# Kernel optimization log

Measured on AMD Instinct MI355X. Metric: run time of the kernel, lower is better.

## Reference

```python
import jax, jax.numpy as jnp
import numpy as np

B, T, F = 4096, 64, 32
U1, U2 = 256, 128  # stacked GRU: rnn_units, rnn_units // 2


def _gru_layer(x, Wg, bg, Wc, bc, units):
    """TF GRUCell semantics over a full sequence.
    x: [B, T, D]. Wg: [D+U, 2U], Wc: [D+U, U]. Returns outputs [B, T, U].
    r,u = sigmoid([x,h] Wg + bg); c = tanh([x, r*h] Wc + bc); h' = u*h + (1-u)*c
    """
    xT = jnp.swapaxes(x, 0, 1)  # [T, B, D]
    h0 = jnp.zeros((x.shape[0], units), x.dtype)

    def step(h, xt):
        gates = jax.nn.sigmoid(jnp.concatenate([xt, h], axis=-1) @ Wg + bg)
        r, u = jnp.split(gates, 2, axis=-1)
        c = jnp.tanh(jnp.concatenate([xt, r * h], axis=-1) @ Wc + bc)
        h_new = u * h + (1.0 - u) * c
        return h_new, h_new

    _, outs = jax.lax.scan(step, h0, xT)
    return jnp.swapaxes(outs, 0, 1)  # [B, T, U]


def setup_inputs() -> dict:
    key = jax.random.key(0)
    ks = jax.random.split(key, 12)
    s = 0.1
    inp = {
        "frames": jax.random.normal(ks[0], (B, T, F), jnp.float32),
        "W1_g": jax.random.normal(ks[1], (F + U1, 2 * U1), jnp.float32) * s,
        "b1_g": jnp.ones((2 * U1,), jnp.float32),  # TF gate bias init = 1.0
        "W1_c": jax.random.normal(ks[2], (F + U1, U1), jnp.float32) * s,
        "b1_c": jnp.zeros((U1,), jnp.float32),
        "W2_g": jax.random.normal(ks[3], (U1 + U2, 2 * U2), jnp.float32) * s,
        "b2_g": jnp.ones((2 * U2,), jnp.float32),
        "W2_c": jax.random.normal(ks[4], (U1 + U2, U2), jnp.float32) * s,
        "b2_c": jnp.zeros((U2,), jnp.float32),
        "Wd": jax.random.normal(ks[5], (U2, F), jnp.float32) * s,
        "bd": jnp.zeros((F,), jnp.float32),
    }
    return inp


def reference(frames, W1_g, b1_g, W1_c, b1_c, W2_g, b2_g, W2_c, b2_c, Wd, bd):
    # stacked GRU: MultiRNNCell([GRUCell(U1), GRUCell(U1 // 2)])
    h1 = _gru_layer(frames, W1_g, b1_g, W1_c, b1_c, U1)   # [B, T, U1]
    h2 = _gru_layer(h1, W2_g, b2_g, W2_c, b2_c, U2)       # [B, T, U2]
    last = h2[:, -1]                                       # use_cell_state=False -> outputs[:, -1]
    predicted = last @ Wd + bd                             # dense to sensor_count
    return predicted
```

## Files before the change

kernel.cpp:

```cpp
#include <hip/hip_runtime.h>


typedef unsigned short u16;
typedef __attribute__((ext_vector_type(8))) short bhalf8;
typedef __attribute__((ext_vector_type(4))) float fx4;

constexpr int Bc = 4096, Tc = 64, Fc = 32, U1 = 256, U2 = 128;
constexpr int K1 = Fc + U1;
constexpr int K2 = U1 + U2;
constexpr int NB = 16, NTHR = 512;
constexpr int LD1 = K1 + 8;
constexpr int LD2 = K2 + 8;

constexpr int nW1g = K1 * 512, nW1c = K1 * 256, nW2g = K2 * 256, nW2c = K2 * 128;
constexpr int oW1g = 0;
constexpr int oW1c = oW1g + nW1g;
constexpr int oW2g = oW1c + nW1c;
constexpr int oW2c = oW2g + nW2g;
constexpr int WTOT = oW2c + nW2c;
constexpr int nWdT = Fc * U2;

#define LGKM_BARRIER() asm volatile("s_waitcnt lgkmcnt(0)\n\ts_barrier" ::: "memory")

__device__ __forceinline__ u16 bf16_rne(float x) {
  unsigned u = __float_as_uint(x);
  return (u16)((u + 0x7fffu + ((u >> 16) & 1u)) >> 16);
}
__device__ __forceinline__ float bf16_f(u16 h) {
  return __uint_as_float(((unsigned)h) << 16);
}
__device__ __forceinline__ float sigm(float x) { return 1.0f / (1.0f + __expf(-x)); }
__device__ __forceinline__ float tanh_(float x) {
  x = fminf(fmaxf(x, -15.0f), 15.0f);
  const float s = __expf(2.0f * x);
  return (s - 1.0f) / (s + 1.0f);
}

__global__ void prep_weights(const float* __restrict__ W1g, const float* __restrict__ W1c,
                             const float* __restrict__ W2g, const float* __restrict__ W2c,
                             const float* __restrict__ Wd, u16* __restrict__ ws) {
  int j = blockIdx.x * 256 + threadIdx.x;
  if (j >= WTOT + nWdT) return;
  if (j >= WTOT) {
    const int jj = j - WTOT;
    float* wdT = (float*)(ws + WTOT);
    const int o = jj >> 7, c = jj & 127;
    wdT[jj] = Wd[c * Fc + o];
    return;
  }
  const float* src; u16* dst; int K, N, jj;
  if (j < nW1g)                    { src = W1g; K = K1; N = 512; jj = j;                      dst = ws + oW1g; }
  else if (j < nW1g + nW1c)        { src = W1c; K = K1; N = 256; jj = j - nW1g;               dst = ws + oW1c; }
  else if (j < nW1g + nW1c + nW2g) { src = W2g; K = K2; N = 256; jj = j - nW1g - nW1c;        dst = ws + oW2g; }
  else                             { src = W2c; K = K2; N = 128; jj = j - nW1g - nW1c - nW2g; dst = ws + oW2c; }
  int n = jj / K, k = jj - n * K;
  dst[(size_t)n * K + k] = bf16_rne(src[(size_t)k * N + n]);
}

template <int NT, int D>
struct Pipe {
  const u16* wp[NT];
  bhalf8 bb[D][NT];
  __device__ __forceinline__ void init(const u16* __restrict__ W, const int* n0,
                                       int K, int lc, int ao) {
#pragma unroll
    for (int i = 0; i < NT; ++i) wp[i] = W + (size_t)(n0[i] + lc) * K + ao;
  }
  __device__ __forceinline__ void prefetch() {
#pragma unroll
    for (int d = 0; d < D; ++d)
#pragma unroll
      for (int i = 0; i < NT; ++i) bb[d][i] = *(const bhalf8*)(wp[i] + d * 32);
  }
  template <int KT, int LDA>
  __device__ __forceinline__ void mm(fx4 (&acc)[NT], const u16 (&Ah)[16][LDA],
                                     const u16 (&Al)[16][LDA], int lc, int ao) {
#pragma unroll
    for (int kt = 0; kt < KT; ++kt) {
      const int k0 = kt * 32;
      const bhalf8 a_h = *(const bhalf8*)&Ah[lc][k0 + ao];
      const bhalf8 a_l = *(const bhalf8*)&Al[lc][k0 + ao];
#pragma unroll
      for (int i = 0; i < NT; ++i) {
        acc[i] = __builtin_amdgcn_mfma_f32_16x16x32_bf16(a_h, bb[kt % D][i], acc[i], 0, 0, 0);
        acc[i] = __builtin_amdgcn_mfma_f32_16x16x32_bf16(a_l, bb[kt % D][i], acc[i], 0, 0, 0);
      }
      if (kt + D < KT) {
#pragma unroll
        for (int i = 0; i < NT; ++i) bb[kt % D][i] = *(const bhalf8*)(wp[i] + (kt + D) * 32);
      }
    }
  }
};

__global__ __launch_bounds__(NTHR, 2)
void gru_mfma(const float* __restrict__ frames, const u16* __restrict__ ws,
              const float* __restrict__ b1g, const float* __restrict__ b1c,
              const float* __restrict__ b2g, const float* __restrict__ b2c,
              const float* __restrict__ bd, float* __restrict__ out) {
  __shared__ alignas(16) u16 A1h[16][LD1], A1l[16][LD1];
  __shared__ alignas(16) u16 A2h[16][LD2], A2l[16][LD2];

  const int tid = threadIdx.x;
  const int w = tid >> 6;
  const int l = tid & 63;
  const int lc = l & 15;
  const int lk = l >> 4;
  const int ao = lk * 8;
  const int row0 = lk * 4;
  const int b0 = blockIdx.x * NB;

  const float bg1r0 = b1g[w * 32 + lc],       bg1r1 = b1g[w * 32 + 16 + lc];
  const float bg1u0 = b1g[256 + w * 32 + lc], bg1u1 = b1g[256 + w * 32 + 16 + lc];
  const float bc10  = b1c[w * 32 + lc],       bc11  = b1c[w * 32 + 16 + lc];
  const float bg2r  = b2g[w * 16 + lc],       bg2u  = b2g[128 + w * 16 + lc];
  const float bc2v  = b2c[w * 16 + lc];

  Pipe<4, 4> pG1;  Pipe<2, 4> pC1;  Pipe<2, 4> pG2;  Pipe<1, 4> pC2;
  const int n0g1[4] = {w * 32, w * 32 + 16, 256 + w * 32, 256 + w * 32 + 16};
  const int n0c1[2] = {w * 32, w * 32 + 16};
  const int n0g2[2] = {w * 16, 128 + w * 16};
  const int n0c2[1] = {w * 16};
  pG1.init(ws + oW1g, n0g1, K1, lc, ao);
  pC1.init(ws + oW1c, n0c1, K1, lc, ao);
  pG2.init(ws + oW2g, n0g2, K2, lc, ao);
  pC2.init(ws + oW2c, n0c2, K2, lc, ao);

  for (int i = tid; i < 16 * LD1; i += NTHR) { (&A1h[0][0])[i] = 0; (&A1l[0][0])[i] = 0; }
  for (int i = tid; i < 16 * LD2; i += NTHR) { (&A2h[0][0])[i] = 0; (&A2l[0][0])[i] = 0; }

  const int xb = tid >> 5, xf = tid & 31;
  const float* fptr = frames + (size_t)(b0 + xb) * (Tc * Fc) + xf;

  {
    const float x0 = fptr[0];
    const u16 h = bf16_rne(x0);
    A1h[xb][xf] = h;
    A1l[xb][xf] = bf16_rne(x0 - bf16_f(h));
  }
  pG1.prefetch();
  LGKM_BARRIER();

  for (int t = 0; t < Tc; ++t) {
    const float xnxt = (t + 1 < Tc) ? fptr[(t + 1) * Fc] : 0.0f;

    fx4 acc[4] = { {bg1r0, bg1r0, bg1r0, bg1r0}, {bg1r1, bg1r1, bg1r1, bg1r1},
                   {bg1u0, bg1u0, bg1u0, bg1u0}, {bg1u1, bg1u1, bg1u1, bg1u1} };
    pG1.mm<9, LD1>(acc, A1h, A1l, lc, ao);
    pC1.prefetch();

    float hold1[2][4];
#pragma unroll
    for (int i = 0; i < 2; ++i)
#pragma unroll
      for (int q = 0; q < 4; ++q) {
        const int row = row0 + q, col = w * 32 + i * 16 + lc;
        hold1[i][q] = bf16_f(A1h[row][Fc + col]) + bf16_f(A1l[row][Fc + col]);
      }
    float rr[2][4], uu[2][4];
#pragma unroll
    for (int i = 0; i < 2; ++i)
#pragma unroll
      for (int q = 0; q < 4; ++q) { rr[i][q] = sigm(acc[i][q]); uu[i][q] = sigm(acc[2 + i][q]); }
    LGKM_BARRIER();

#pragma unroll
    for (int i = 0; i < 2; ++i)
#pragma unroll
      for (int q = 0; q < 4; ++q) {
        const int row = row0 + q, col = w * 32 + i * 16 + lc;
        const float rh = rr[i][q] * hold1[i][q];
        const u16 hh = bf16_rne(rh);
        A1h[row][Fc + col] = hh;
        A1l[row][Fc + col] = bf16_rne(rh - bf16_f(hh));
      }
    LGKM_BARRIER();

    fx4 accc[2] = { {bc10, bc10, bc10, bc10}, {bc11, bc11, bc11, bc11} };
    pC1.mm<9, LD1>(accc, A1h, A1l, lc, ao);
    pG2.prefetch();

    float hn1[2][4]; u16 hh1[2][4], hl1[2][4];
#pragma unroll
    for (int i = 0; i < 2; ++i)
#pragma unroll
      for (int q = 0; q < 4; ++q) {
        const float c = tanh_(accc[i][q]);
        const float hn = c + uu[i][q] * (hold1[i][q] - c);
        hh1[i][q] = bf16_rne(hn);
        hl1[i][q] = bf16_rne(hn - bf16_f(hh1[i][q]));
      }
    LGKM_BARRIER();
#pragma unroll
    for (int i = 0; i < 2; ++i)
#pragma unroll
      for (int q = 0; q < 4; ++q) {
        const int row = row0 + q, col = w * 32 + i * 16 + lc;
        A1h[row][Fc + col] = hh1[i][q];  A1l[row][Fc + col] = hl1[i][q];
        A2h[row][col] = hh1[i][q];       A2l[row][col] = hl1[i][q];
      }
    LGKM_BARRIER();

    fx4 acc2[2] = { {bg2r, bg2r, bg2r, bg2r}, {bg2u, bg2u, bg2u, bg2u} };
    pG2.mm<12, LD2>(acc2, A2h, A2l, lc, ao);
    pC2.prefetch();

    float hold2[4];
#pragma unroll
    for (int q = 0; q < 4; ++q) {
      const int row = row0 + q, col = w * 16 + lc;
      hold2[q] = bf16_f(A2h[row][U1 + col]) + bf16_f(A2l[row][U1 + col]);
    }
    float rr2[4], uu2[4];
#pragma unroll
    for (int q = 0; q < 4; ++q) { rr2[q] = sigm(acc2[0][q]); uu2[q] = sigm(acc2[1][q]); }
    LGKM_BARRIER();

#pragma unroll
    for (int q = 0; q < 4; ++q) {
      const int row = row0 + q, col = w * 16 + lc;
      const float rh = rr2[q] * hold2[q];
      const u16 hh = bf16_rne(rh);
      A2h[row][U1 + col] = hh;
      A2l[row][U1 + col] = bf16_rne(rh - bf16_f(hh));
    }
    LGKM_BARRIER();

    fx4 acc3[1] = { {bc2v, bc2v, bc2v, bc2v} };
    pC2.mm<12, LD2>(acc3, A2h, A2l, lc, ao);
    pG1.prefetch();
    LGKM_BARRIER();

#pragma unroll
    for (int q = 0; q < 4; ++q) {
      const int row = row0 + q, col = w * 16 + lc;
      const float c = tanh_(acc3[0][q]);
      const float hn = c + uu2[q] * (hold2[q] - c);
      const u16 hh = bf16_rne(hn);
      A2h[row][U1 + col] = hh;
      A2l[row][U1 + col] = bf16_rne(hn - bf16_f(hh));
    }
    {
      const u16 h = bf16_rne(xnxt);
      A1h[xb][xf] = h;
      A1l[xb][xf] = bf16_rne(xnxt - bf16_f(h));
    }
    LGKM_BARRIER();
  }

  {
    const float* wdT = (const float*)(ws + WTOT);
    const int o = tid & 31, b = tid >> 5;
    const float4* wrow = (const float4*)(wdT + o * 128);
    float acc = bd[o];
#pragma unroll 8
    for (int c4 = 0; c4 < 32; ++c4) {
      const float4 wv = wrow[c4];
      const int c = c4 * 4;
      const float h0 = bf16_f(A2h[b][U1 + c + 0]) + bf16_f(A2l[b][U1 + c + 0]);
      const float h1 = bf16_f(A2h[b][U1 + c + 1]) + bf16_f(A2l[b][U1 + c + 1]);
      const float h2 = bf16_f(A2h[b][U1 + c + 2]) + bf16_f(A2l[b][U1 + c + 2]);
      const float h3 = bf16_f(A2h[b][U1 + c + 3]) + bf16_f(A2l[b][U1 + c + 3]);
      acc = fmaf(h0, wv.x, fmaf(h1, wv.y, fmaf(h2, wv.z, fmaf(h3, wv.w, acc))));
    }
    out[(size_t)(b0 + b) * Fc + o] = acc;
  }
}

extern "C" void kernel_launch(void* const* d_in, const int* in_sizes, int n_in,
                              void* d_out, int out_size, void* d_ws, size_t ws_size,
                              hipStream_t stream) {
  const float* frames = (const float*)d_in[0];
  const float* W1g = (const float*)d_in[1];
  const float* b1g = (const float*)d_in[2];
  const float* W1c = (const float*)d_in[3];
  const float* b1c = (const float*)d_in[4];
  const float* W2g = (const float*)d_in[5];
  const float* b2g = (const float*)d_in[6];
  const float* W2c = (const float*)d_in[7];
  const float* b2c = (const float*)d_in[8];
  const float* Wd  = (const float*)d_in[9];
  const float* bd  = (const float*)d_in[10];
  u16* ws = (u16*)d_ws;
  float* outp = (float*)d_out;

  hipLaunchKernelGGL(prep_weights, dim3((WTOT + nWdT + 255) / 256), dim3(256), 0, stream,
                     W1g, W1c, W2g, W2c, Wd, ws);
  hipLaunchKernelGGL(gru_mfma, dim3(Bc / NB), dim3(NTHR), 0, stream,
                     frames, ws, b1g, b1c, b2g, b2c, bd, outp);
}
```

Measured before the change: 881.1 us.

## Process 32 batch rows per block with XOR-swizzled LDS and weight-fragment reuse

Doubles the batch rows per block from 16 to 32, so each weight fragment loaded from global memory feeds two MFMA row tiles. This halves weight traffic per sample and halves the block count to 128. LDS moves to dynamic shared memory with an XOR swizzle to avoid bank conflicts, and the prefetch depths for several matmuls are deepened. The costs are fewer blocks than CUs, more registers, and a larger LDS footprint, which can lower occupancy.

```diff
diff --git a/kernel.cpp b/kernel.cpp
--- a/kernel.cpp
+++ b/kernel.cpp
@@ -3,14 +3,16 @@
 
 typedef unsigned short u16;
 typedef __attribute__((ext_vector_type(8))) short bhalf8;
+typedef __attribute__((ext_vector_type(8))) short short8;
 typedef __attribute__((ext_vector_type(4))) float fx4;
 
 constexpr int Bc = 4096, Tc = 64, Fc = 32, U1 = 256, U2 = 128;
 constexpr int K1 = Fc + U1;
 constexpr int K2 = U1 + U2;
-constexpr int NB = 16, NTHR = 512;
-constexpr int LD1 = K1 + 8;
-constexpr int LD2 = K2 + 8;
+constexpr int NB = 32, NTHR = 512;
+constexpr int NBLK = Bc / NB;
+constexpr int LD1 = 320;
+constexpr int LD2 = 384;
 
 constexpr int nW1g = K1 * 512, nW1c = K1 * 256, nW2g = K2 * 256, nW2c = K2 * 128;
 constexpr int oW1g = 0;
@@ -20,7 +22,16 @@
 constexpr int WTOT = oW2c + nW2c;
 constexpr int nWdT = Fc * U2;
 
+constexpr int SM_A1 = 32 * LD1;
+constexpr int SM_A2 = 32 * LD2;
+constexpr int SMEM_U16 = 2 * SM_A1 + 2 * SM_A2;
+constexpr size_t SMEM_BYTES = (size_t)SMEM_U16 * 2;
+
 #define LGKM_BARRIER() asm volatile("s_waitcnt lgkmcnt(0)\n\ts_barrier" ::: "memory")
+
+__device__ __forceinline__ int swz(int row, int col, int LDA) {
+  return row * LDA + (col ^ ((row & 7) << 3));
+}
 
 __device__ __forceinline__ u16 bf16_rne(float x) {
   unsigned u = __float_as_uint(x);
@@ -73,17 +84,25 @@
       for (int i = 0; i < NT; ++i) bb[d][i] = *(const bhalf8*)(wp[i] + d * 32);
   }
   template <int KT, int LDA>
-  __device__ __forceinline__ void mm(fx4 (&acc)[NT], const u16 (&Ah)[16][LDA],
-                                     const u16 (&Al)[16][LDA], int lc, int ao) {
+  __device__ __forceinline__ void mm2(fx4 (&acc)[NT][2], const u16* __restrict__ Ah,
+                                      const u16* __restrict__ Al, int lc, int ao) {
 #pragma unroll
     for (int kt = 0; kt < KT; ++kt) {
-      const int k0 = kt * 32;
-      const bhalf8 a_h = *(const bhalf8*)&Ah[lc][k0 + ao];
-      const bhalf8 a_l = *(const bhalf8*)&Al[lc][k0 + ao];
+      const int c0 = kt * 32 + ao;
+      const int cs = c0 ^ ((lc & 7) << 3);
+      const int i0 = lc * LDA + cs;
+      const int i1 = (lc + 16) * LDA + cs;
+      const bhalf8 ah0 = *(const bhalf8*)&Ah[i0];
+      const bhalf8 al0 = *(const bhalf8*)&Al[i0];
+      const bhalf8 ah1 = *(const bhalf8*)&Ah[i1];
+      const bhalf8 al1 = *(const bhalf8*)&Al[i1];
 #pragma unroll
       for (int i = 0; i < NT; ++i) {
-        acc[i] = __builtin_amdgcn_mfma_f32_16x16x32_bf16(a_h, bb[kt % D][i], acc[i], 0, 0, 0);
-        acc[i] = __builtin_amdgcn_mfma_f32_16x16x32_bf16(a_l, bb[kt % D][i], acc[i], 0, 0, 0);
+        const bhalf8 b = bb[kt % D][i];
+        acc[i][0] = __builtin_amdgcn_mfma_f32_16x16x32_bf16(ah0, b, acc[i][0], 0, 0, 0);
+        acc[i][0] = __builtin_amdgcn_mfma_f32_16x16x32_bf16(al0, b, acc[i][0], 0, 0, 0);
+        acc[i][1] = __builtin_amdgcn_mfma_f32_16x16x32_bf16(ah1, b, acc[i][1], 0, 0, 0);
+        acc[i][1] = __builtin_amdgcn_mfma_f32_16x16x32_bf16(al1, b, acc[i][1], 0, 0, 0);
       }
       if (kt + D < KT) {
 #pragma unroll
@@ -98,8 +117,11 @@
               const float* __restrict__ b1g, const float* __restrict__ b1c,
               const float* __restrict__ b2g, const float* __restrict__ b2c,
               const float* __restrict__ bd, float* __restrict__ out) {
-  __shared__ alignas(16) u16 A1h[16][LD1], A1l[16][LD1];
-  __shared__ alignas(16) u16 A2h[16][LD2], A2l[16][LD2];
+  extern __shared__ u16 smem[];
+  u16* A1h = smem;
+  u16* A1l = A1h + SM_A1;
+  u16* A2h = A1l + SM_A1;
+  u16* A2l = A2h + SM_A2;
 
   const int tid = threadIdx.x;
   const int w = tid >> 6;
@@ -116,7 +138,7 @@
   const float bg2r  = b2g[w * 16 + lc],       bg2u  = b2g[128 + w * 16 + lc];
   const float bc2v  = b2c[w * 16 + lc];
 
-  Pipe<4, 4> pG1;  Pipe<2, 4> pC1;  Pipe<2, 4> pG2;  Pipe<1, 4> pC2;
+  Pipe<4, 4> pG1;  Pipe<2, 6> pC1;  Pipe<2, 6> pG2;  Pipe<1, 8> pC2;
   const int n0g1[4] = {w * 32, w * 32 + 16, 256 + w * 32, 256 + w * 32 + 16};
   const int n0c1[2] = {w * 32, w * 32 + 16};
   const int n0g2[2] = {w * 16, 128 + w * 16};
@@ -126,144 +148,188 @@
   pG2.init(ws + oW2g, n0g2, K2, lc, ao);
   pC2.init(ws + oW2c, n0c2, K2, lc, ao);
 
-  for (int i = tid; i < 16 * LD1; i += NTHR) { (&A1h[0][0])[i] = 0; (&A1l[0][0])[i] = 0; }
-  for (int i = tid; i < 16 * LD2; i += NTHR) { (&A2h[0][0])[i] = 0; (&A2l[0][0])[i] = 0; }
-
-  const int xb = tid >> 5, xf = tid & 31;
-  const float* fptr = frames + (size_t)(b0 + xb) * (Tc * Fc) + xf;
+  for (int i = tid; i < SMEM_U16; i += NTHR) smem[i] = 0;
+
+  const int xb = tid >> 4;
+  const int xf0 = (tid & 15) * 2;
+  const float* fptr = frames + (size_t)(b0 + xb) * (Tc * Fc) + xf0;
 
   {
-    const float x0 = fptr[0];
-    const u16 h = bf16_rne(x0);
-    A1h[xb][xf] = h;
-    A1l[xb][xf] = bf16_rne(x0 - bf16_f(h));
+    const float2 x0 = *(const float2*)(fptr);
+    const u16 h0 = bf16_rne(x0.x), h1 = bf16_rne(x0.y);
+    const u16 l0 = bf16_rne(x0.x - bf16_f(h0)), l1 = bf16_rne(x0.y - bf16_f(h1));
+    const int idx = swz(xb, xf0, LD1);
+    *(unsigned*)&A1h[idx] = (unsigned)h0 | ((unsigned)h1 << 16);
+    *(unsigned*)&A1l[idx] = (unsigned)l0 | ((unsigned)l1 << 16);
   }
   pG1.prefetch();
   LGKM_BARRIER();
 
   for (int t = 0; t < Tc; ++t) {
-    const float xnxt = (t + 1 < Tc) ? fptr[(t + 1) * Fc] : 0.0f;
-
-    fx4 acc[4] = { {bg1r0, bg1r0, bg1r0, bg1r0}, {bg1r1, bg1r1, bg1r1, bg1r1},
-                   {bg1u0, bg1u0, bg1u0, bg1u0}, {bg1u1, bg1u1, bg1u1, bg1u1} };
-    pG1.mm<9, LD1>(acc, A1h, A1l, lc, ao);
+    const float2 xn = (t + 1 < Tc) ? *(const float2*)(fptr + (t + 1) * Fc)
+                                   : make_float2(0.0f, 0.0f);
+
+    fx4 a1[4][2] = {
+      { {bg1r0, bg1r0, bg1r0, bg1r0}, {bg1r0, bg1r0, bg1r0, bg1r0} },
+      { {bg1r1, bg1r1, bg1r1, bg1r1}, {bg1r1, bg1r1, bg1r1, bg1r1} },
+      { {bg1u0, bg1u0, bg1u0, bg1u0}, {bg1u0, bg1u0, bg1u0, bg1u0} },
+      { {bg1u1, bg1u1, bg1u1, bg1u1}, {bg1u1, bg1u1, bg1u1, bg1u1} } };
+    pG1.mm2<9, LD1>(a1, A1h, A1l, lc, ao);
     pC1.prefetch();
 
-    float hold1[2][4];
-#pragma unroll
-    for (int i = 0; i < 2; ++i)
+    float hold1[2][2][4];
+#pragma unroll
+    for (int m = 0; m < 2; ++m)
+#pragma unroll
+      for (int i = 0; i < 2; ++i)
+#pragma unroll
+        for (int q = 0; q < 4; ++q) {
+          const int idx = swz(16 * m + row0 + q, Fc + w * 32 + i * 16 + lc, LD1);
+          hold1[m][i][q] = bf16_f(A1h[idx]) + bf16_f(A1l[idx]);
+        }
+    float rr[2][2][4], uu[2][2][4];
+#pragma unroll
+    for (int m = 0; m < 2; ++m)
+#pragma unroll
+      for (int i = 0; i < 2; ++i)
+#pragma unroll
+        for (int q = 0; q < 4; ++q) {
+          rr[m][i][q] = sigm(a1[i][m][q]);
+          uu[m][i][q] = sigm(a1[2 + i][m][q]);
+        }
+    LGKM_BARRIER();
+
+#pragma unroll
+    for (int m = 0; m < 2; ++m)
+#pragma unroll
+      for (int i = 0; i < 2; ++i)
+#pragma unroll
+        for (int q = 0; q < 4; ++q) {
+          const int idx = swz(16 * m + row0 + q, Fc + w * 32 + i * 16 + lc, LD1);
+          const float rh = rr[m][i][q] * hold1[m][i][q];
+          const u16 hh = bf16_rne(rh);
+          A1h[idx] = hh;
+          A1l[idx] = bf16_rne(rh - bf16_f(hh));
+        }
+    LGKM_BARRIER();
+
+    fx4 c1a[2][2] = {
+      { {bc10, bc10, bc10, bc10}, {bc10, bc10, bc10, bc10} },
+      { {bc11, bc11, bc11, bc11}, {bc11, bc11, bc11, bc11} } };
+    pC1.mm2<9, LD1>(c1a, A1h, A1l, lc, ao);
+    pG2.prefetch();
+
+    u16 hh1[2][2][4], hl1[2][2][4];
+#pragma unroll
+    for (int m = 0; m < 2; ++m)
+#pragma unroll
+      for (int i = 0; i < 2; ++i)
+#pragma unroll
+        for (int q = 0; q < 4; ++q) {
+          const float c = tanh_(c1a[i][m][q]);
+          const float hn = c + uu[m][i][q] * (hold1[m][i][q] - c);
+          hh1[m][i][q] = bf16_rne(hn);
+          hl1[m][i][q] = bf16_rne(hn - bf16_f(hh1[m][i][q]));
+        }
+    LGKM_BARRIER();
+#pragma unroll
+    for (int m = 0; m < 2; ++m)
+#pragma unroll
+      for (int i = 0; i < 2; ++i)
+#pragma unroll
+        for (int q = 0; q < 4; ++q) {
+          const int row = 16 * m + row0 + q, col = w * 32 + i * 16 + lc;
+          const int idx1 = swz(row, Fc + col, LD1);
+          A1h[idx1] = hh1[m][i][q];  A1l[idx1] = hl1[m][i][q];
+          const int idx2 = swz(row, col, LD2);
+          A2h[idx2] = hh1[m][i][q];  A2l[idx2] = hl1[m][i][q];
+        }
+    LGKM_BARRIER();
+
+    fx4 a2[2][2] = {
+      { {bg2r, bg2r, bg2r, bg2r}, {bg2r, bg2r, bg2r, bg2r} },
+      { {bg2u, bg2u, bg2u, bg2u}, {bg2u, bg2u, bg2u, bg2u} } };
+    pG2.mm2<12, LD2>(a2, A2h, A2l, lc, ao);
+    pC2.prefetch();
+
+    float hold2[2][4];
+#pragma unroll
+    for (int m = 0; m < 2; ++m)
 #pragma unroll
       for (int q = 0; q < 4; ++q) {
-        const int row = row0 + q, col = w * 32 + i * 16 + lc;
-        hold1[i][q] = bf16_f(A1h[row][Fc + col]) + bf16_f(A1l[row][Fc + col]);
-      }
-    float rr[2][4], uu[2][4];
-#pragma unroll
-    for (int i = 0; i < 2; ++i)
-#pragma unroll
-      for (int q = 0; q < 4; ++q) { rr[i][q] = sigm(acc[i][q]); uu[i][q] = sigm(acc[2 + i][q]); }
-    LGKM_BARRIER();
-
-#pragma unroll
-    for (int i = 0; i < 2; ++i)
+        const int idx = swz(16 * m + row0 + q, U1 + w * 16 + lc, LD2);
+        hold2[m][q] = bf16_f(A2h[idx]) + bf16_f(A2l[idx]);
+      }
+    float rr2[2][4], uu2[2][4];
+#pragma unroll
+    for (int m = 0; m < 2; ++m)
 #pragma unroll
       for (int q = 0; q < 4; ++q) {
-        const int row = row0 + q, col = w * 32 + i * 16 + lc;
-        const float rh = rr[i][q] * hold1[i][q];
+        rr2[m][q] = sigm(a2[0][m][q]);
+        uu2[m][q] = sigm(a2[1][m][q]);
+      }
+    LGKM_BARRIER();
+
+#pragma unroll
+    for (int m = 0; m < 2; ++m)
+#pragma unroll
+      for (int q = 0; q < 4; ++q) {
+        const int idx = swz(16 * m + row0 + q, U1 + w * 16 + lc, LD2);
+        const float rh = rr2[m][q] * hold2[m][q];
         const u16 hh = bf16_rne(rh);
-        A1h[row][Fc + col] = hh;
-        A1l[row][Fc + col] = bf16_rne(rh - bf16_f(hh));
-      }
-    LGKM_BARRIER();
-
-    fx4 accc[2] = { {bc10, bc10, bc10, bc10}, {bc11, bc11, bc11, bc11} };
-    pC1.mm<9, LD1>(accc, A1h, A1l, lc, ao);
-    pG2.prefetch();
-
-    float hn1[2][4]; u16 hh1[2][4], hl1[2][4];
-#pragma unroll
-    for (int i = 0; i < 2; ++i)
+        A2h[idx] = hh;
+        A2l[idx] = bf16_rne(rh - bf16_f(hh));
+      }
+    LGKM_BARRIER();
+
+    fx4 c2a[1][2] = { { {bc2v, bc2v, bc2v, bc2v}, {bc2v, bc2v, bc2v, bc2v} } };
+    pC2.mm2<12, LD2>(c2a, A2h, A2l, lc, ao);
+    pG1.prefetch();
+    LGKM_BARRIER();
+
+#pragma unroll
+    for (int m = 0; m < 2; ++m)
 #pragma unroll
       for (int q = 0; q < 4; ++q) {
-        const float c = tanh_(accc[i][q]);
-        const float hn = c + uu[i][q] * (hold1[i][q] - c);
-        hh1[i][q] = bf16_rne(hn);
-        hl1[i][q] = bf16_rne(hn - bf16_f(hh1[i][q]));
-      }
-    LGKM_BARRIER();
-#pragma unroll
-    for (int i = 0; i < 2; ++i)
-#pragma unroll
-      for (int q = 0; q < 4; ++q) {
-        const int row = row0 + q, col = w * 32 + i * 16 + lc;
-        A1h[row][Fc + col] = hh1[i][q];  A1l[row][Fc + col] = hl1[i][q];
-        A2h[row][col] = hh1[i][q];       A2l[row][col] = hl1[i][q];
-      }
-    LGKM_BARRIER();
-
-    fx4 acc2[2] = { {bg2r, bg2r, bg2r, bg2r}, {bg2u, bg2u, bg2u, bg2u} };
-    pG2.mm<12, LD2>(acc2, A2h, A2l, lc, ao);
-    pC2.prefetch();
-
-    float hold2[4];
-#pragma unroll
-    for (int q = 0; q < 4; ++q) {
-      const int row = row0 + q, col = w * 16 + lc;
-      hold2[q] = bf16_f(A2h[row][U1 + col]) + bf16_f(A2l[row][U1 + col]);
-    }
-    float rr2[4], uu2[4];
-#pragma unroll
-    for (int q = 0; q < 4; ++q) { rr2[q] = sigm(acc2[0][q]); uu2[q] = sigm(acc2[1][q]); }
-    LGKM_BARRIER();
-
-#pragma unroll
-    for (int q = 0; q < 4; ++q) {
-      const int row = row0 + q, col = w * 16 + lc;
-      const float rh = rr2[q] * hold2[q];
-      const u16 hh = bf16_rne(rh);
-      A2h[row][U1 + col] = hh;
-      A2l[row][U1 + col] = bf16_rne(rh - bf16_f(hh));
-    }
-    LGKM_BARRIER();
-
-    fx4 acc3[1] = { {bc2v, bc2v, bc2v, bc2v} };
-    pC2.mm<12, LD2>(acc3, A2h, A2l, lc, ao);
-    pG1.prefetch();
-    LGKM_BARRIER();
-
-#pragma unroll
-    for (int q = 0; q < 4; ++q) {
-      const int row = row0 + q, col = w * 16 + lc;
-      const float c = tanh_(acc3[0][q]);
-      const float hn = c + uu2[q] * (hold2[q] - c);
-      const u16 hh = bf16_rne(hn);
-      A2h[row][U1 + col] = hh;
-      A2l[row][U1 + col] = bf16_rne(hn - bf16_f(hh));
-    }
+        const int idx = swz(16 * m + row0 + q, U1 + w * 16 + lc, LD2);
+        const float c = tanh_(c2a[0][m][q]);
+        const float hn = c + uu2[m][q] * (hold2[m][q] - c);
+        const u16 hh = bf16_rne(hn);
+        A2h[idx] = hh;
+        A2l[idx] = bf16_rne(hn - bf16_f(hh));
+      }
     {
-      const u16 h = bf16_rne(xnxt);
-      A1h[xb][xf] = h;
-      A1l[xb][xf] = bf16_rne(xnxt - bf16_f(h));
+      const u16 h0 = bf16_rne(xn.x), h1 = bf16_rne(xn.y);
+      const u16 l0 = bf16_rne(xn.x - bf16_f(h0)), l1 = bf16_rne(xn.y - bf16_f(h1));
+      const int idx = swz(xb, xf0, LD1);
+      *(unsigned*)&A1h[idx] = (unsigned)h0 | ((unsigned)h1 << 16);
+      *(unsigned*)&A1l[idx] = (unsigned)l0 | ((unsigned)l1 << 16);
     }
     LGKM_BARRIER();
   }
 
   {
     const float* wdT = (const float*)(ws + WTOT);
-    const int o = tid & 31, b = tid >> 5;
-    const float4* wrow = (const float4*)(wdT + o * 128);
-    float acc = bd[o];
-#pragma unroll 8
-    for (int c4 = 0; c4 < 32; ++c4) {
-      const float4 wv = wrow[c4];
-      const int c = c4 * 4;
-      const float h0 = bf16_f(A2h[b][U1 + c + 0]) + bf16_f(A2l[b][U1 + c + 0]);
-      const float h1 = bf16_f(A2h[b][U1 + c + 1]) + bf16_f(A2l[b][U1 + c + 1]);
-      const float h2 = bf16_f(A2h[b][U1 + c + 2]) + bf16_f(A2l[b][U1 + c + 2]);
-      const float h3 = bf16_f(A2h[b][U1 + c + 3]) + bf16_f(A2l[b][U1 + c + 3]);
-      acc = fmaf(h0, wv.x, fmaf(h1, wv.y, fmaf(h2, wv.z, fmaf(h3, wv.w, acc))));
+    const int o = tid & 31, bq = tid >> 5;
+    float accA = bd[o], accB = bd[o];
+#pragma unroll 4
+    for (int c8 = 0; c8 < 16; ++c8) {
+      const int c = c8 * 8;
+      const int ia = swz(bq, U1 + c, LD2);
+      const int ib = swz(bq + 16, U1 + c, LD2);
+      const short8 vhA = *(const short8*)&A2h[ia];
+      const short8 vlA = *(const short8*)&A2l[ia];
+      const short8 vhB = *(const short8*)&A2h[ib];
+      const short8 vlB = *(const short8*)&A2l[ib];
+#pragma unroll
+      for (int j = 0; j < 8; ++j) {
+        const float wv = wdT[o * 128 + c + j];
+        accA = fmaf(bf16_f((u16)vhA[j]) + bf16_f((u16)vlA[j]), wv, accA);
+        accB = fmaf(bf16_f((u16)vhB[j]) + bf16_f((u16)vlB[j]), wv, accB);
+      }
     }
-    out[(size_t)(b0 + b) * Fc + o] = acc;
+    out[(size_t)(b0 + bq) * Fc + o] = accA;
+    out[(size_t)(b0 + bq + 16) * Fc + o] = accB;
   }
 }
 
@@ -284,8 +350,15 @@
   u16* ws = (u16*)d_ws;
   float* outp = (float*)d_out;
 
+  static bool attr_set = false;
+  if (!attr_set) {
+    hipFuncSetAttribute(reinterpret_cast<const void*>(gru_mfma),
+                        hipFuncAttributeMaxDynamicSharedMemorySize, (int)SMEM_BYTES);
+    attr_set = true;
+  }
+
   hipLaunchKernelGGL(prep_weights, dim3((WTOT + nWdT + 255) / 256), dim3(256), 0, stream,
                      W1g, W1c, W2g, W2c, Wd, ws);
-  hipLaunchKernelGGL(gru_mfma, dim3(Bc / NB), dim3(NTHR), 0, stream,
+  hipLaunchKernelGGL(gru_mfma, dim3(NBLK), dim3(NTHR), SMEM_BYTES, stream,
                      frames, ws, b1g, b1c, b2g, b2c, bd, outp);
 }
```

New measurement: 2.662 ms. 3.02x slower.

## Switch GRU kernel to 32x32x16 MFMA with 32-row batch tiles and swizzled shared layout

Applied to the files above, without the earlier changes.

Doubles the batch tile per block to 32 rows and uses 32x32x16 bf16 MFMA instructions, so each weight fragment loaded from global memory is reused across twice as many batch rows. Layer-1 hidden state now lives in the same XOR-swizzled shared buffer as layer-2 input, which removes the duplicate h1 copy and is meant to avoid LDS bank conflicts. Layer-2 gate work is split across warps by r/u halves, and only half the warps run the candidate matmul. This halves the grid to 128 blocks at one block per CU, which risks leaving CUs idle and offers less latency hiding.

```diff
diff --git a/kernel.cpp b/kernel.cpp
--- a/kernel.cpp
+++ b/kernel.cpp
@@ -3,14 +3,16 @@
 
 typedef unsigned short u16;
 typedef __attribute__((ext_vector_type(8))) short bhalf8;
-typedef __attribute__((ext_vector_type(4))) float fx4;
+typedef __attribute__((ext_vector_type(8))) short short8;
+typedef __attribute__((ext_vector_type(16))) float fx16;
 
 constexpr int Bc = 4096, Tc = 64, Fc = 32, U1 = 256, U2 = 128;
 constexpr int K1 = Fc + U1;
 constexpr int K2 = U1 + U2;
-constexpr int NB = 16, NTHR = 512;
-constexpr int LD1 = K1 + 8;
-constexpr int LD2 = K2 + 8;
+constexpr int NB = 32, NTHR = 512;
+constexpr int NBLK = Bc / NB;
+constexpr int LDX = 40;
+constexpr int LD2 = 384;
 
 constexpr int nW1g = K1 * 512, nW1c = K1 * 256, nW2g = K2 * 256, nW2c = K2 * 128;
 constexpr int oW1g = 0;
@@ -57,213 +59,264 @@
   dst[(size_t)n * K + k] = bf16_rne(src[(size_t)k * N + n]);
 }
 
-template <int NT, int D>
+template <int NT, int D, int KH>
 struct Pipe {
   const u16* wp[NT];
   bhalf8 bb[D][NT];
   __device__ __forceinline__ void init(const u16* __restrict__ W, const int* n0,
-                                       int K, int lc, int ao) {
-#pragma unroll
-    for (int i = 0; i < NT; ++i) wp[i] = W + (size_t)(n0[i] + lc) * K + ao;
+                                       int K, int cl, int ko) {
+#pragma unroll
+    for (int i = 0; i < NT; ++i) wp[i] = W + (size_t)(n0[i] + cl) * K + ko;
   }
   __device__ __forceinline__ void prefetch() {
 #pragma unroll
     for (int d = 0; d < D; ++d)
 #pragma unroll
-      for (int i = 0; i < NT; ++i) bb[d][i] = *(const bhalf8*)(wp[i] + d * 32);
-  }
-  template <int KT, int LDA>
-  __device__ __forceinline__ void mm(fx4 (&acc)[NT], const u16 (&Ah)[16][LDA],
-                                     const u16 (&Al)[16][LDA], int lc, int ao) {
-#pragma unroll
-    for (int kt = 0; kt < KT; ++kt) {
-      const int k0 = kt * 32;
-      const bhalf8 a_h = *(const bhalf8*)&Ah[lc][k0 + ao];
-      const bhalf8 a_l = *(const bhalf8*)&Al[lc][k0 + ao];
-#pragma unroll
-      for (int i = 0; i < NT; ++i) {
-        acc[i] = __builtin_amdgcn_mfma_f32_16x16x32_bf16(a_h, bb[kt % D][i], acc[i], 0, 0, 0);
-        acc[i] = __builtin_amdgcn_mfma_f32_16x16x32_bf16(a_l, bb[kt % D][i], acc[i], 0, 0, 0);
-      }
-      if (kt + D < KT) {
-#pragma unroll
-        for (int i = 0; i < NT; ++i) bb[kt % D][i] = *(const bhalf8*)(wp[i] + (kt + D) * 32);
-      }
+      for (int i = 0; i < NT; ++i) bb[d][i] = *(const bhalf8*)(wp[i] + d * 16);
+  }
+  __device__ __forceinline__ void roll(int kh) {
+    if (kh + D < KH) {
+#pragma unroll
+      for (int i = 0; i < NT; ++i) bb[kh % D][i] = *(const bhalf8*)(wp[i] + (kh + D) * 16);
     }
   }
 };
 
-__global__ __launch_bounds__(NTHR, 2)
+__global__ __launch_bounds__(NTHR, 1)
 void gru_mfma(const float* __restrict__ frames, const u16* __restrict__ ws,
               const float* __restrict__ b1g, const float* __restrict__ b1c,
               const float* __restrict__ b2g, const float* __restrict__ b2c,
               const float* __restrict__ bd, float* __restrict__ out) {
-  __shared__ alignas(16) u16 A1h[16][LD1], A1l[16][LD1];
-  __shared__ alignas(16) u16 A2h[16][LD2], A2l[16][LD2];
+  __shared__ alignas(16) u16 A2h_s[32 * LD2], A2l_s[32 * LD2];
+  __shared__ alignas(16) u16 A1xh[32 * LDX], A1xl[32 * LDX];
 
   const int tid = threadIdx.x;
   const int w = tid >> 6;
   const int l = tid & 63;
-  const int lc = l & 15;
-  const int lk = l >> 4;
-  const int ao = lk * 8;
-  const int row0 = lk * 4;
+  const int cl = l & 31;
+  const int hi = l >> 5;
+  const int ko = hi * 8;
   const int b0 = blockIdx.x * NB;
 
-  const float bg1r0 = b1g[w * 32 + lc],       bg1r1 = b1g[w * 32 + 16 + lc];
-  const float bg1u0 = b1g[256 + w * 32 + lc], bg1u1 = b1g[256 + w * 32 + 16 + lc];
-  const float bc10  = b1c[w * 32 + lc],       bc11  = b1c[w * 32 + 16 + lc];
-  const float bg2r  = b2g[w * 16 + lc],       bg2u  = b2g[128 + w * 16 + lc];
-  const float bc2v  = b2c[w * 16 + lc];
-
-  Pipe<4, 4> pG1;  Pipe<2, 4> pC1;  Pipe<2, 4> pG2;  Pipe<1, 4> pC2;
-  const int n0g1[4] = {w * 32, w * 32 + 16, 256 + w * 32, 256 + w * 32 + 16};
-  const int n0c1[2] = {w * 32, w * 32 + 16};
-  const int n0g2[2] = {w * 16, 128 + w * 16};
-  const int n0c2[1] = {w * 16};
-  pG1.init(ws + oW1g, n0g1, K1, lc, ao);
-  pC1.init(ws + oW1c, n0c1, K1, lc, ao);
-  pG2.init(ws + oW2g, n0g2, K2, lc, ao);
-  pC2.init(ws + oW2c, n0c2, K2, lc, ao);
-
-  for (int i = tid; i < 16 * LD1; i += NTHR) { (&A1h[0][0])[i] = 0; (&A1l[0][0])[i] = 0; }
-  for (int i = tid; i < 16 * LD2; i += NTHR) { (&A2h[0][0])[i] = 0; (&A2l[0][0])[i] = 0; }
-
-  const int xb = tid >> 5, xf = tid & 31;
-  const float* fptr = frames + (size_t)(b0 + xb) * (Tc * Fc) + xf;
+  const int col1 = w * 32 + cl;
+  const int w2 = (w < 4) ? w : (w - 4);
+  const int col2 = w2 * 32 + cl;
+
+  const float bR  = b1g[col1];
+  const float bU  = b1g[256 + col1];
+  const float bC1 = b1c[col1];
+  const float bG2 = (w < 4) ? b2g[128 + col2] : b2g[col2];
+  const float bC2 = b2c[col2];
+
+  Pipe<2, 4, 18> pG1;  Pipe<1, 6, 18> pC1;  Pipe<1, 6, 24> pG2;  Pipe<1, 6, 24> pC2;
+  const int n0g1[2] = {w * 32, 256 + w * 32};
+  const int n0c1[1] = {w * 32};
+  const int n0g2[1] = {(w < 4) ? (128 + w * 32) : ((w - 4) * 32)};
+  const int n0c2[1] = {w2 * 32};
+  pG1.init(ws + oW1g, n0g1, K1, cl, ko);
+  pC1.init(ws + oW1c, n0c1, K1, cl, ko);
+  pG2.init(ws + oW2g, n0g2, K2, cl, ko);
+  pC2.init(ws + oW2c, n0c2, K2, cl, ko);
+
+  for (int i = tid; i < 32 * LD2; i += NTHR) { A2h_s[i] = 0; A2l_s[i] = 0; }
+  for (int i = tid; i < 32 * LDX; i += NTHR) { A1xh[i] = 0; A1xl[i] = 0; }
+
+  const int xb = tid >> 4;
+  const int xf0 = (tid & 15) * 2;
+  const float* fptr = frames + (size_t)(b0 + xb) * (Tc * Fc) + xf0;
 
   {
-    const float x0 = fptr[0];
-    const u16 h = bf16_rne(x0);
-    A1h[xb][xf] = h;
-    A1l[xb][xf] = bf16_rne(x0 - bf16_f(h));
+    const float2 x0 = *(const float2*)(fptr);
+    const u16 h0 = bf16_rne(x0.x), h1v = bf16_rne(x0.y);
+    const u16 l0 = bf16_rne(x0.x - bf16_f(h0)), l1v = bf16_rne(x0.y - bf16_f(h1v));
+    const int idx = xb * LDX + xf0;
+    *(unsigned*)&A1xh[idx] = (unsigned)h0 | ((unsigned)h1v << 16);
+    *(unsigned*)&A1xl[idx] = (unsigned)l0 | ((unsigned)l1v << 16);
   }
   pG1.prefetch();
   LGKM_BARRIER();
 
+  auto ldA1 = [&](int kh, bhalf8& ah, bhalf8& al) {
+    if (kh < 2) {
+      const int idx = cl * LDX + kh * 16 + ko;
+      ah = *(const bhalf8*)&A1xh[idx];
+      al = *(const bhalf8*)&A1xl[idx];
+    } else {
+      const int c = kh * 16 - 32 + ko;
+      const int idx = cl * LD2 + (c ^ ((cl & 7) << 3));
+      ah = *(const bhalf8*)&A2h_s[idx];
+      al = *(const bhalf8*)&A2l_s[idx];
+    }
+  };
+  auto ldA2 = [&](int kh, bhalf8& ah, bhalf8& al) {
+    const int c = kh * 16 + ko;
+    const int idx = cl * LD2 + (c ^ ((cl & 7) << 3));
+    ah = *(const bhalf8*)&A2h_s[idx];
+    al = *(const bhalf8*)&A2l_s[idx];
+  };
+  auto ew = [&](int row, int col) { return row * LD2 + (col ^ ((row & 7) << 3)); };
+
   for (int t = 0; t < Tc; ++t) {
-    const float xnxt = (t + 1 < Tc) ? fptr[(t + 1) * Fc] : 0.0f;
-
-    fx4 acc[4] = { {bg1r0, bg1r0, bg1r0, bg1r0}, {bg1r1, bg1r1, bg1r1, bg1r1},
-                   {bg1u0, bg1u0, bg1u0, bg1u0}, {bg1u1, bg1u1, bg1u1, bg1u1} };
-    pG1.mm<9, LD1>(acc, A1h, A1l, lc, ao);
+    const float2 xn = (t + 1 < Tc) ? *(const float2*)(fptr + (t + 1) * Fc)
+                                   : make_float2(0.0f, 0.0f);
+
+    fx16 aR, aU;
+#pragma unroll
+    for (int j = 0; j < 16; ++j) { aR[j] = bR; aU[j] = bU; }
+#pragma unroll
+    for (int kh = 0; kh < 18; ++kh) {
+      bhalf8 ah, al; ldA1(kh, ah, al);
+      aR = __builtin_amdgcn_mfma_f32_32x32x16_bf16(ah, pG1.bb[kh % 4][0], aR, 0, 0, 0);
+      aR = __builtin_amdgcn_mfma_f32_32x32x16_bf16(al, pG1.bb[kh % 4][0], aR, 0, 0, 0);
+      aU = __builtin_amdgcn_mfma_f32_32x32x16_bf16(ah, pG1.bb[kh % 4][1], aU, 0, 0, 0);
+      aU = __builtin_amdgcn_mfma_f32_32x32x16_bf16(al, pG1.bb[kh % 4][1], aU, 0, 0, 0);
+      pG1.roll(kh);
+    }
     pC1.prefetch();
 
-    float hold1[2][4];
-#pragma unroll
-    for (int i = 0; i < 2; ++i)
-#pragma unroll
-      for (int q = 0; q < 4; ++q) {
-        const int row = row0 + q, col = w * 32 + i * 16 + lc;
-        hold1[i][q] = bf16_f(A1h[row][Fc + col]) + bf16_f(A1l[row][Fc + col]);
+    float hold1[16], rr[16], uu[16];
+#pragma unroll
+    for (int j = 0; j < 16; ++j) {
+      const int row = (j & 3) + 8 * (j >> 2) + 4 * hi;
+      const int idx = ew(row, col1);
+      hold1[j] = bf16_f(A2h_s[idx]) + bf16_f(A2l_s[idx]);
+      rr[j] = sigm(aR[j]);
+      uu[j] = sigm(aU[j]);
+    }
+    LGKM_BARRIER();
+#pragma unroll
+    for (int j = 0; j < 16; ++j) {
+      const int row = (j & 3) + 8 * (j >> 2) + 4 * hi;
+      const int idx = ew(row, col1);
+      const float rh = rr[j] * hold1[j];
+      const u16 hh = bf16_rne(rh);
+      A2h_s[idx] = hh;
+      A2l_s[idx] = bf16_rne(rh - bf16_f(hh));
+    }
+    LGKM_BARRIER();
+
+    fx16 aC;
+#pragma unroll
+    for (int j = 0; j < 16; ++j) aC[j] = bC1;
+#pragma unroll
+    for (int kh = 0; kh < 18; ++kh) {
+      bhalf8 ah, al; ldA1(kh, ah, al);
+      aC = __builtin_amdgcn_mfma_f32_32x32x16_bf16(ah, pC1.bb[kh % 6][0], aC, 0, 0, 0);
+      aC = __builtin_amdgcn_mfma_f32_32x32x16_bf16(al, pC1.bb[kh % 6][0], aC, 0, 0, 0);
+      pC1.roll(kh);
+    }
+    pG2.prefetch();
+
+    u16 hh1[16], hl1[16];
+#pragma unroll
+    for (int j = 0; j < 16; ++j) {
+      const float c = tanh_(aC[j]);
+      const float hn = c + uu[j] * (hold1[j] - c);
+      hh1[j] = bf16_rne(hn);
+      hl1[j] = bf16_rne(hn - bf16_f(hh1[j]));
+    }
+    LGKM_BARRIER();
+#pragma unroll
+    for (int j = 0; j < 16; ++j) {
+      const int row = (j & 3) + 8 * (j >> 2) + 4 * hi;
+      const int idx = ew(row, col1);
+      A2h_s[idx] = hh1[j];
+      A2l_s[idx] = hl1[j];
+    }
+    {
+      const u16 h0 = bf16_rne(xn.x), h1v = bf16_rne(xn.y);
+      const u16 l0 = bf16_rne(xn.x - bf16_f(h0)), l1v = bf16_rne(xn.y - bf16_f(h1v));
+      const int idx = xb * LDX + xf0;
+      *(unsigned*)&A1xh[idx] = (unsigned)h0 | ((unsigned)h1v << 16);
+      *(unsigned*)&A1xl[idx] = (unsigned)l0 | ((unsigned)l1v << 16);
+    }
+    LGKM_BARRIER();
+
+    fx16 a2;
+#pragma unroll
+    for (int j = 0; j < 16; ++j) a2[j] = bG2;
+#pragma unroll
+    for (int kh = 0; kh < 24; ++kh) {
+      bhalf8 ah, al; ldA2(kh, ah, al);
+      a2 = __builtin_amdgcn_mfma_f32_32x32x16_bf16(ah, pG2.bb[kh % 6][0], a2, 0, 0, 0);
+      a2 = __builtin_amdgcn_mfma_f32_32x32x16_bf16(al, pG2.bb[kh % 6][0], a2, 0, 0, 0);
+      pG2.roll(kh);
+    }
+    if (w < 4) pC2.prefetch();
+
+    float hold2[16], g2v[16];
+#pragma unroll
+    for (int j = 0; j < 16; ++j) {
+      const int row = (j & 3) + 8 * (j >> 2) + 4 * hi;
+      const int idx = ew(row, 256 + col2);
+      hold2[j] = bf16_f(A2h_s[idx]) + bf16_f(A2l_s[idx]);
+      g2v[j] = sigm(a2[j]);
+    }
+    LGKM_BARRIER();
+    if (w >= 4) {
+#pragma unroll
+      for (int j = 0; j < 16; ++j) {
+        const int row = (j & 3) + 8 * (j >> 2) + 4 * hi;
+        const int idx = ew(row, 256 + col2);
+        const float rh = g2v[j] * hold2[j];
+        const u16 hh = bf16_rne(rh);
+        A2h_s[idx] = hh;
+        A2l_s[idx] = bf16_rne(rh - bf16_f(hh));
       }
-    float rr[2][4], uu[2][4];
-#pragma unroll
-    for (int i = 0; i < 2; ++i)
-#pragma unroll
-      for (int q = 0; q < 4; ++q) { rr[i][q] = sigm(acc[i][q]); uu[i][q] = sigm(acc[2 + i][q]); }
-    LGKM_BARRIER();
-
-#pragma unroll
-    for (int i = 0; i < 2; ++i)
-#pragma unroll
-      for (int q = 0; q < 4; ++q) {
-        const int row = row0 + q, col = w * 32 + i * 16 + lc;
-        const float rh = rr[i][q] * hold1[i][q];
-        const u16 hh = bf16_rne(rh);
-        A1h[row][Fc + col] = hh;
-        A1l[row][Fc + col] = bf16_rne(rh - bf16_f(hh));
+    }
+    LGKM_BARRIER();
+
+    fx16 aC2;
+#pragma unroll
+    for (int j = 0; j < 16; ++j) aC2[j] = bC2;
+    if (w < 4) {
+#pragma unroll
+      for (int kh = 0; kh < 24; ++kh) {
+        bhalf8 ah, al; ldA2(kh, ah, al);
+        aC2 = __builtin_amdgcn_mfma_f32_32x32x16_bf16(ah, pC2.bb[kh % 6][0], aC2, 0, 0, 0);
+        aC2 = __builtin_amdgcn_mfma_f32_32x32x16_bf16(al, pC2.bb[kh % 6][0], aC2, 0, 0, 0);
+        pC2.roll(kh);
       }
-    LGKM_BARRIER();
-
-    fx4 accc[2] = { {bc10, bc10, bc10, bc10}, {bc11, bc11, bc11, bc11} };
-    pC1.mm<9, LD1>(accc, A1h, A1l, lc, ao);
-    pG2.prefetch();
-
-    float hn1[2][4]; u16 hh1[2][4], hl1[2][4];
-#pragma unroll
-    for (int i = 0; i < 2; ++i)
-#pragma unroll
-      for (int q = 0; q < 4; ++q) {
-        const float c = tanh_(accc[i][q]);
-        const float hn = c + uu[i][q] * (hold1[i][q] - c);
-        hh1[i][q] = bf16_rne(hn);
-        hl1[i][q] = bf16_rne(hn - bf16_f(hh1[i][q]));
+    }
+    pG1.prefetch();
+    LGKM_BARRIER();
+    if (w < 4) {
+#pragma unroll
+      for (int j = 0; j < 16; ++j) {
+        const int row = (j & 3) + 8 * (j >> 2) + 4 * hi;
+        const int idx = ew(row, 256 + col2);
+        const float c = tanh_(aC2[j]);
+        const float hn = c + g2v[j] * (hold2[j] - c);
+        const u16 hh = bf16_rne(hn);
+        A2h_s[idx] = hh;
+        A2l_s[idx] = bf16_rne(hn - bf16_f(hh));
       }
-    LGKM_BARRIER();
-#pragma unroll
-    for (int i = 0; i < 2; ++i)
-#pragma unroll
-      for (int q = 0; q < 4; ++q) {
-        const int row = row0 + q, col = w * 32 + i * 16 + lc;
-        A1h[row][Fc + col] = hh1[i][q];  A1l[row][Fc + col] = hl1[i][q];
-        A2h[row][col] = hh1[i][q];       A2l[row][col] = hl1[i][q];
-      }
-    LGKM_BARRIER();
-
-    fx4 acc2[2] = { {bg2r, bg2r, bg2r, bg2r}, {bg2u, bg2u, bg2u, bg2u} };
-    pG2.mm<12, LD2>(acc2, A2h, A2l, lc, ao);
-    pC2.prefetch();
-
-    float hold2[4];
-#pragma unroll
-    for (int q = 0; q < 4; ++q) {
-      const int row = row0 + q, col = w * 16 + lc;
-      hold2[q] = bf16_f(A2h[row][U1 + col]) + bf16_f(A2l[row][U1 + col]);
-    }
-    float rr2[4], uu2[4];
-#pragma unroll
-    for (int q = 0; q < 4; ++q) { rr2[q] = sigm(acc2[0][q]); uu2[q] = sigm(acc2[1][q]); }
-    LGKM_BARRIER();
-
-#pragma unroll
-    for (int q = 0; q < 4; ++q) {
-      const int row = row0 + q, col = w * 16 + lc;
-      const float rh = rr2[q] * hold2[q];
-      const u16 hh = bf16_rne(rh);
-      A2h[row][U1 + col] = hh;
-      A2l[row][U1 + col] = bf16_rne(rh - bf16_f(hh));
-    }
-    LGKM_BARRIER();
-
-    fx4 acc3[1] = { {bc2v, bc2v, bc2v, bc2v} };
-    pC2.mm<12, LD2>(acc3, A2h, A2l, lc, ao);
-    pG1.prefetch();
-    LGKM_BARRIER();
-
-#pragma unroll
-    for (int q = 0; q < 4; ++q) {
-      const int row = row0 + q, col = w * 16 + lc;
-      const float c = tanh_(acc3[0][q]);
-      const float hn = c + uu2[q] * (hold2[q] - c);
-      const u16 hh = bf16_rne(hn);
-      A2h[row][U1 + col] = hh;
-      A2l[row][U1 + col] = bf16_rne(hn - bf16_f(hh));
-    }
-    {
-      const u16 h = bf16_rne(xnxt);
-      A1h[xb][xf] = h;
-      A1l[xb][xf] = bf16_rne(xnxt - bf16_f(h));
     }
     LGKM_BARRIER();
   }
 
   {
     const float* wdT = (const float*)(ws + WTOT);
-    const int o = tid & 31, b = tid >> 5;
-    const float4* wrow = (const float4*)(wdT + o * 128);
-    float acc = bd[o];
-#pragma unroll 8
-    for (int c4 = 0; c4 < 32; ++c4) {
-      const float4 wv = wrow[c4];
-      const int c = c4 * 4;
-      const float h0 = bf16_f(A2h[b][U1 + c + 0]) + bf16_f(A2l[b][U1 + c + 0]);
-      const float h1 = bf16_f(A2h[b][U1 + c + 1]) + bf16_f(A2l[b][U1 + c + 1]);
-      const float h2 = bf16_f(A2h[b][U1 + c + 2]) + bf16_f(A2l[b][U1 + c + 2]);
-      const float h3 = bf16_f(A2h[b][U1 + c + 3]) + bf16_f(A2l[b][U1 + c + 3]);
-      acc = fmaf(h0, wv.x, fmaf(h1, wv.y, fmaf(h2, wv.z, fmaf(h3, wv.w, acc))));
-    }
-    out[(size_t)(b0 + b) * Fc + o] = acc;
+    const int o = tid & 31, bq = tid >> 5;
+    float accA = bd[o], accB = bd[o];
+#pragma unroll 4
+    for (int c8 = 0; c8 < 16; ++c8) {
+      const int c = c8 * 8;
+      const int ia = ew(bq, 256 + c);
+      const int ib = ew(bq + 16, 256 + c);
+      const short8 vhA = *(const short8*)&A2h_s[ia];
+      const short8 vlA = *(const short8*)&A2l_s[ia];
+      const short8 vhB = *(const short8*)&A2h_s[ib];
+      const short8 vlB = *(const short8*)&A2l_s[ib];
+#pragma unroll
+      for (int j = 0; j < 8; ++j) {
+        const float wv = wdT[o * 128 + c + j];
+        accA = fmaf(bf16_f((u16)vhA[j]) + bf16_f((u16)vlA[j]), wv, accA);
+        accB = fmaf(bf16_f((u16)vhB[j]) + bf16_f((u16)vlB[j]), wv, accB);
+      }
+    }
+    out[(size_t)(b0 + bq) * Fc + o] = accA;
+    out[(size_t)(b0 + bq + 16) * Fc + o] = accB;
   }
 }
 
@@ -286,6 +339,6 @@
 
   hipLaunchKernelGGL(prep_weights, dim3((WTOT + nWdT + 255) / 256), dim3(256), 0, stream,
                      W1g, W1c, W2g, W2c, Wd, ws);
-  hipLaunchKernelGGL(gru_mfma, dim3(Bc / NB), dim3(NTHR), 0, stream,
+  hipLaunchKernelGGL(gru_mfma, dim3(NBLK), dim3(NTHR), 0, stream,
                      frames, ws, b1g, b1c, b2g, b2c, bd, outp);
 }
```

Measured after the change: 2.148 ms. +143.8%, slower.
